# Performance work log

Hardware: AMD Instinct MI355X
Metric: run time of the kernel (lower is better)

The kernel has to match this reference:

```python
import jax, jax.numpy as jnp
import numpy as np

B, L = 256, 32768

def _avg_pool1d(x, k, p):
    # count_include_pad=True avg pool via prefix sums: O(L) instead of O(L*k)
    xp = jnp.pad(x, ((0, 0), (0, 0), (p, p)))
    cs = jnp.cumsum(xp, axis=-1)
    cs = jnp.pad(cs, ((0, 0), (0, 0), (1, 0)))  # leading zero for window diff
    return (cs[..., k:] - cs[..., :-k]) / k

def setup_inputs() -> dict:
    key = jax.random.key(0)
    x = jax.random.normal(key, (B, L), dtype=jnp.float32)
    return {"x": x}

def reference(x):
    x = x[:, None, :]  # [B, 1, L]
    # log(max(1, 1+x)) and log(max(1, 1-x)): cat-with-ones + max == clamp at 1
    a = jnp.log(jnp.maximum(1.0, 1.0 + x))
    b = jnp.log(jnp.maximum(1.0, 1.0 - x))
    a0 = _avg_pool1d(a, 3, 1)
    a5 = _avg_pool1d(a, 199, 99)
    b0 = _avg_pool1d(b, 3, 1)
    b5 = _avg_pool1d(b, 199, 99)
    return jnp.concatenate([a0 - a5, a0, b0 - b5, b0], axis=1)  # [B, 4, L]
```

## Files before the change

### kernel.cpp

```cpp
#include <hip/hip_runtime.h>

#define B_DIM 256
#define L_DIM 32768
#define CHUNK 2048
#define HALO  100
#define NTOT  (CHUNK + 2*HALO)
#define NG    (NTOT/4)
#define T     256
#define EPT   9

typedef float fx4 __attribute__((ext_vector_type(4)));

__global__ __launch_bounds__(T) void pool_feat_kernel(const float* __restrict__ x,
                                                      float* __restrict__ out) {
    const int row    = blockIdx.y;
    const int chunk0 = blockIdx.x * CHUNK;
    const int tid    = threadIdx.x;

    __shared__ __align__(16) float sA[NTOT];
    __shared__ __align__(16) float sB[NTOT];
    __shared__ float waveA[4];
    __shared__ float waveB[4];

    const float* xr = x + (size_t)row * L_DIM;

    for (int g = tid; g < NG; g += T) {
        const int c = chunk0 - HALO + 4 * g;
        fx4 v;
        if (c >= 0 && c + 3 < L_DIM) {
            v = *reinterpret_cast<const fx4*>(xr + c);
        } else {
            v.x = (c + 0 >= 0 && c + 0 < L_DIM) ? xr[c + 0] : 0.0f;
            v.y = (c + 1 >= 0 && c + 1 < L_DIM) ? xr[c + 1] : 0.0f;
            v.z = (c + 2 >= 0 && c + 2 < L_DIM) ? xr[c + 2] : 0.0f;
            v.w = (c + 3 >= 0 && c + 3 < L_DIM) ? xr[c + 3] : 0.0f;
        }
        *reinterpret_cast<fx4*>(&sA[4 * g]) = v;
    }
    __syncthreads();

    const int s0 = tid * EPT;
    float ra[EPT], rb[EPT];
    float runA = 0.0f, runB = 0.0f;
    #pragma unroll
    for (int j = 0; j < EPT; ++j) {
        const int idx = s0 + j;
        const float v = (idx < NTOT) ? sA[idx] : 0.0f;
        runA += __logf(fmaxf(1.0f, 1.0f + v));
        runB += __logf(fmaxf(1.0f, 1.0f - v));
        ra[j] = runA; rb[j] = runB;
    }

    float vA = runA, vB = runB;
    const int lane = tid & 63;
    const int wid  = tid >> 6;
    #pragma unroll
    for (int d = 1; d < 64; d <<= 1) {
        float uA = __shfl_up(vA, d);
        float uB = __shfl_up(vB, d);
        if (lane >= d) { vA += uA; vB += uB; }
    }
    if (lane == 63) { waveA[wid] = vA; waveB[wid] = vB; }
    __syncthreads();
    float offA = vA - runA;
    float offB = vB - runB;
    #pragma unroll
    for (int w = 0; w < 3; ++w) {
        if (w < wid) { offA += waveA[w]; offB += waveB[w]; }
    }

    #pragma unroll
    for (int j = 0; j < EPT; ++j) {
        const int idx = s0 + j;
        if (idx < NTOT) { sA[idx] = ra[j] + offA; sB[idx] = rb[j] + offB; }
    }
    __syncthreads();

    const float inv3   = 1.0f / 3.0f;
    const float inv199 = 1.0f / 199.0f;
    float* ob = out + (size_t)row * 4u * L_DIM + chunk0;
    #pragma unroll
    for (int it = 0; it < CHUNK / (4 * T); ++it) {
        const int i0 = 4 * (tid + it * T);
        fx4 r0, r1, r2, r3;
        #pragma unroll
        for (int arr = 0; arr < 2; ++arr) {
            const float* s = arr ? sB : sA;
            const fx4 L0 = *reinterpret_cast<const fx4*>(s + i0);
            const fx4 L1 = *reinterpret_cast<const fx4*>(s + i0 + 96);
            const fx4 L2 = *reinterpret_cast<const fx4*>(s + i0 + 100);
            const fx4 L3 = *reinterpret_cast<const fx4*>(s + i0 + 104);
            const fx4 L4 = *reinterpret_cast<const fx4*>(s + i0 + 196);
            const fx4 L5 = *reinterpret_cast<const fx4*>(s + i0 + 200);
            const float csI[4]   = {L0.x, L0.y, L0.z, L0.w};
            const float cs98[4]  = {L1.z, L1.w, L2.x, L2.y};
            const float cs101[4] = {L2.y, L2.z, L2.w, L3.x};
            const float cs199[4] = {L4.w, L5.x, L5.y, L5.z};
            fx4& rs = arr ? r3 : r1;
            fx4& rd = arr ? r2 : r0;
            #pragma unroll
            for (int u = 0; u < 4; ++u) {
                const float p0 = (cs101[u] - cs98[u]) * inv3;
                const float p5 = (cs199[u] - csI[u]) * inv199;
                rs[u] = p0;
                rd[u] = p0 - p5;
            }
        }
        __builtin_nontemporal_store(r0, reinterpret_cast<fx4*>(ob + 0 * (size_t)L_DIM + i0));
        __builtin_nontemporal_store(r1, reinterpret_cast<fx4*>(ob + 1 * (size_t)L_DIM + i0));
        __builtin_nontemporal_store(r2, reinterpret_cast<fx4*>(ob + 2 * (size_t)L_DIM + i0));
        __builtin_nontemporal_store(r3, reinterpret_cast<fx4*>(ob + 3 * (size_t)L_DIM + i0));
    }
}

extern "C" void kernel_launch(void* const* d_in, const int* in_sizes, int n_in,
                              void* d_out, int out_size, void* d_ws, size_t ws_size,
                              hipStream_t stream) {
    const float* x = (const float*)d_in[0];
    float* out = (float*)d_out;
    dim3 grid(L_DIM / CHUNK, B_DIM);
    pool_feat_kernel<<<grid, dim3(T), 0, stream>>>(x, out);
}
```

Measured before the change: 32.27 us.

## Double chunk size, recompute logs instead of holding prefix registers, 8-wide outputs

Chunk grows to 4096 elements with 512 threads, padding shared memory to T*EPT so bounds checks disappear and halo overhead per output shrinks. The second pass recomputes the log terms from shared memory instead of keeping per-thread prefix arrays in registers, which lowers register pressure at the cost of doubled transcendental work. Each thread now produces 8 contiguous outputs per array in one pass, reusing overlapping shared loads. Half as many blocks are launched, which may reduce occupancy and parallelism.

```diff
diff --git a/kernel.cpp b/kernel.cpp
--- a/kernel.cpp
+++ b/kernel.cpp
@@ -2,12 +2,14 @@
 
 #define B_DIM 256
 #define L_DIM 32768
-#define CHUNK 2048
+#define CHUNK 4096
 #define HALO  100
-#define NTOT  (CHUNK + 2*HALO)
-#define NG    (NTOT/4)
-#define T     256
+#define NREAL (CHUNK + 2*HALO)
+#define T     512
 #define EPT   9
+#define NPAD  (T*EPT)
+#define NG    (NPAD/4)
+#define NWAVE (T/64)
 
 typedef float fx4 __attribute__((ext_vector_type(4)));
 
@@ -17,10 +19,10 @@
     const int chunk0 = blockIdx.x * CHUNK;
     const int tid    = threadIdx.x;
 
-    __shared__ __align__(16) float sA[NTOT];
-    __shared__ __align__(16) float sB[NTOT];
-    __shared__ float waveA[4];
-    __shared__ float waveB[4];
+    __shared__ __align__(16) float sA[NPAD];
+    __shared__ __align__(16) float sB[NPAD];
+    __shared__ float waveA[NWAVE];
+    __shared__ float waveB[NWAVE];
 
     const float* xr = x + (size_t)row * L_DIM;
 
@@ -40,15 +42,12 @@
     __syncthreads();
 
     const int s0 = tid * EPT;
-    float ra[EPT], rb[EPT];
     float runA = 0.0f, runB = 0.0f;
     #pragma unroll
     for (int j = 0; j < EPT; ++j) {
-        const int idx = s0 + j;
-        const float v = (idx < NTOT) ? sA[idx] : 0.0f;
+        const float v = sA[s0 + j];
         runA += __logf(fmaxf(1.0f, 1.0f + v));
         runB += __logf(fmaxf(1.0f, 1.0f - v));
-        ra[j] = runA; rb[j] = runB;
     }
 
     float vA = runA, vB = runB;
@@ -65,51 +64,60 @@
     float offA = vA - runA;
     float offB = vB - runB;
     #pragma unroll
-    for (int w = 0; w < 3; ++w) {
+    for (int w = 0; w < NWAVE - 1; ++w) {
         if (w < wid) { offA += waveA[w]; offB += waveB[w]; }
     }
 
+    float accA = offA, accB = offB;
     #pragma unroll
     for (int j = 0; j < EPT; ++j) {
-        const int idx = s0 + j;
-        if (idx < NTOT) { sA[idx] = ra[j] + offA; sB[idx] = rb[j] + offB; }
+        const float v = sA[s0 + j];
+        accA += __logf(fmaxf(1.0f, 1.0f + v));
+        accB += __logf(fmaxf(1.0f, 1.0f - v));
+        sA[s0 + j] = accA;
+        sB[s0 + j] = accB;
     }
     __syncthreads();
 
     const float inv3   = 1.0f / 3.0f;
     const float inv199 = 1.0f / 199.0f;
-    float* ob = out + (size_t)row * 4u * L_DIM + chunk0;
+    const int i0 = 8 * tid;
+    float* ob = out + (size_t)row * 4u * L_DIM + chunk0 + i0;
     #pragma unroll
-    for (int it = 0; it < CHUNK / (4 * T); ++it) {
-        const int i0 = 4 * (tid + it * T);
-        fx4 r0, r1, r2, r3;
+    for (int arr = 0; arr < 2; ++arr) {
+        const float* s = arr ? sB : sA;
+        const fx4 V0 = *reinterpret_cast<const fx4*>(s + i0);
+        const fx4 V1 = *reinterpret_cast<const fx4*>(s + i0 + 4);
+        const fx4 W0 = *reinterpret_cast<const fx4*>(s + i0 + 96);
+        const fx4 W1 = *reinterpret_cast<const fx4*>(s + i0 + 100);
+        const fx4 W2 = *reinterpret_cast<const fx4*>(s + i0 + 104);
+        const fx4 W3 = *reinterpret_cast<const fx4*>(s + i0 + 108);
+        const fx4 X0 = *reinterpret_cast<const fx4*>(s + i0 + 196);
+        const fx4 X1 = *reinterpret_cast<const fx4*>(s + i0 + 200);
+        const fx4 X2 = *reinterpret_cast<const fx4*>(s + i0 + 204);
+        const float csI[8]   = {V0.x,V0.y,V0.z,V0.w, V1.x,V1.y,V1.z,V1.w};
+        const float cs98[8]  = {W0.z,W0.w, W1.x,W1.y,W1.z,W1.w, W2.x,W2.y};
+        const float cs101[8] = {W1.y,W1.z,W1.w, W2.x,W2.y,W2.z,W2.w, W3.x};
+        const float cs199[8] = {X0.w, X1.x,X1.y,X1.z,X1.w, X2.x,X2.y,X2.z};
+        float ps[8], pd[8];
         #pragma unroll
-        for (int arr = 0; arr < 2; ++arr) {
-            const float* s = arr ? sB : sA;
-            const fx4 L0 = *reinterpret_cast<const fx4*>(s + i0);
-            const fx4 L1 = *reinterpret_cast<const fx4*>(s + i0 + 96);
-            const fx4 L2 = *reinterpret_cast<const fx4*>(s + i0 + 100);
-            const fx4 L3 = *reinterpret_cast<const fx4*>(s + i0 + 104);
-            const fx4 L4 = *reinterpret_cast<const fx4*>(s + i0 + 196);
-            const fx4 L5 = *reinterpret_cast<const fx4*>(s + i0 + 200);
-            const float csI[4]   = {L0.x, L0.y, L0.z, L0.w};
-            const float cs98[4]  = {L1.z, L1.w, L2.x, L2.y};
-            const float cs101[4] = {L2.y, L2.z, L2.w, L3.x};
-            const float cs199[4] = {L4.w, L5.x, L5.y, L5.z};
-            fx4& rs = arr ? r3 : r1;
-            fx4& rd = arr ? r2 : r0;
-            #pragma unroll
-            for (int u = 0; u < 4; ++u) {
-                const float p0 = (cs101[u] - cs98[u]) * inv3;
-                const float p5 = (cs199[u] - csI[u]) * inv199;
-                rs[u] = p0;
-                rd[u] = p0 - p5;
-            }
+        for (int u = 0; u < 8; ++u) {
+            const float p0 = (cs101[u] - cs98[u]) * inv3;
+            const float p5 = (cs199[u] - csI[u]) * inv199;
+            ps[u] = p0;
+            pd[u] = p0 - p5;
         }
-        __builtin_nontemporal_store(r0, reinterpret_cast<fx4*>(ob + 0 * (size_t)L_DIM + i0));
-        __builtin_nontemporal_store(r1, reinterpret_cast<fx4*>(ob + 1 * (size_t)L_DIM + i0));
-        __builtin_nontemporal_store(r2, reinterpret_cast<fx4*>(ob + 2 * (size_t)L_DIM + i0));
-        __builtin_nontemporal_store(r3, reinterpret_cast<fx4*>(ob + 3 * (size_t)L_DIM + i0));
+        float* od = ob + (size_t)(arr ? 2 : 0) * L_DIM;
+        float* os = ob + (size_t)(arr ? 3 : 1) * L_DIM;
+        fx4 t;
+        t.x=pd[0]; t.y=pd[1]; t.z=pd[2]; t.w=pd[3];
+        __builtin_nontemporal_store(t, reinterpret_cast<fx4*>(od));
+        t.x=pd[4]; t.y=pd[5]; t.z=pd[6]; t.w=pd[7];
+        __builtin_nontemporal_store(t, reinterpret_cast<fx4*>(od + 4));
+        t.x=ps[0]; t.y=ps[1]; t.z=ps[2]; t.w=ps[3];
+        __builtin_nontemporal_store(t, reinterpret_cast<fx4*>(os));
+        t.x=ps[4]; t.y=ps[5]; t.z=ps[6]; t.w=ps[7];
+        __builtin_nontemporal_store(t, reinterpret_cast<fx4*>(os + 4));
     }
 }
 
```

Result: slower. 59.66 us (+84.9%).
